# Kernel tuning notes

Hardware: AMD Instinct MI355X
Metric: run time of the kernel (lower is better)

## Reference

```python
import jax, jax.numpy as jnp
import numpy as np

N_NODES = 100000
IN_DIM = 128
HID = 128
N_REL = 2
N_EDGES = 500000


def setup_inputs() -> dict:
    key = jax.random.key(0)
    ks = jax.random.split(key, 12)
    x = jax.random.normal(ks[0], (N_NODES, IN_DIM), dtype=jnp.float32)
    edge_index = jax.random.randint(ks[1], (2, N_EDGES), 0, N_NODES, dtype=jnp.int64)
    edge_type = jax.random.randint(ks[2], (N_EDGES,), 0, N_REL, dtype=jnp.int64)
    def w(k, shape, fan_in):
        return jax.random.normal(k, shape, dtype=jnp.float32) / np.sqrt(fan_in)
    return {
        "x": x,
        "edge_index": edge_index,
        "edge_type": edge_type,
        "W_rel1": w(ks[3], (N_REL, IN_DIM, HID), IN_DIM),
        "W_root1": w(ks[4], (IN_DIM, HID), IN_DIM),
        "b1": jnp.zeros((HID,), jnp.float32),
        "W_rel2": w(ks[5], (N_REL, HID, HID), HID),
        "W_root2": w(ks[6], (HID, HID), HID),
        "b2": jnp.zeros((HID,), jnp.float32),
        "Wc": w(ks[7], (HID, 2), HID),
        "bc": jnp.zeros((2,), jnp.float32),
    }


def rgcn_conv(x, src, dst, edge_type, W_rel, W_root, b, n_nodes):
    """PyG RGCNConv: out_i = x_i @ W_root + b + sum_r mean_{j in N_r(i)} x_j @ W_r."""
    out = x @ W_root + b
    for r in range(W_rel.shape[0]):  # small fixed relation count
        mask = (edge_type == r).astype(x.dtype)  # [E]
        xr = x @ W_rel[r]                         # [N, dout] transform-then-gather
        msg = xr[src] * mask[:, None]             # [E, dout]
        agg = jax.ops.segment_sum(msg, dst, num_segments=n_nodes)   # [N, dout]
        cnt = jax.ops.segment_sum(mask, dst, num_segments=n_nodes)  # [N]
        out = out + agg / jnp.maximum(cnt, 1.0)[:, None]            # mean aggr
    return out


def reference(x, edge_index, edge_type, W_rel1, W_root1, b1, W_rel2, W_root2, b2, Wc, bc):
    n = x.shape[0]
    src, dst = edge_index[0], edge_index[1]
    h = rgcn_conv(x, src, dst, edge_type, W_rel1, W_root1, b1, n)
    h = jax.nn.relu(h)
    # dropout is identity at inference (training=False)
    h = rgcn_conv(h, src, dst, edge_type, W_rel2, W_root2, b2, n)
    h = jax.nn.relu(h)
    logits = h @ Wc + bc
    return logits
```

## Files before the change

### kernel.cpp

```cpp
#include <hip/hip_runtime.h>
#include <hip/hip_fp16.h>

#define N_NODES 100000
#define PAD_N   100096
#define IN_DIM 128
#define HID 128
#define N_REL 2
#define N_EDGES 500000
#define M_SEG (N_REL * N_NODES)
#define SCAN_BLK 1024
#define SCAN_NB ((M_SEG + SCAN_BLK - 1) / SCAN_BLK)

#define CVT_BLOCKS 12500
#define PACK_BLOCKS 48
#define HIST_BLOCKS 1954

#define GB_EDGES 48

typedef __attribute__((ext_vector_type(8))) _Float16 half8;
typedef __attribute__((ext_vector_type(4))) float float4v;

__device__ __forceinline__ unsigned short f2h(float f) {
    return __half_as_ushort(__float2half(f));
}

__global__ __launch_bounds__(256) void prep_kernel(
    const float* __restrict__ X, unsigned short* __restrict__ Xb,
    const float* __restrict__ Wroot1, const float* __restrict__ Wrel1,
    const float* __restrict__ Wroot2, const float* __restrict__ Wrel2,
    unsigned short* __restrict__ Wp,
    const int* __restrict__ ei, const int* __restrict__ et,
    unsigned* __restrict__ cnt)
{
    int bid = blockIdx.x;
    if (bid < CVT_BLOCKS) {
        int i = bid * 256 + threadIdx.x;
        if (i >= N_NODES * IN_DIM / 4) return;
        float4 v = ((const float4*)X)[i];
        ushort4 o;
        o.x = f2h(v.x); o.y = f2h(v.y); o.z = f2h(v.z); o.w = f2h(v.w);
        ((ushort4*)Xb)[i] = o;
    } else if (bid < CVT_BLOCKS + PACK_BLOCKS) {
        int tid = (bid - CVT_BLOCKS) * 256 + threadIdx.x;
        int layer = tid / 6144;
        int rem   = tid % 6144;
        int ks    = rem / 512;
        int rem2  = rem % 512;
        int nt    = rem2 / 64;
        int lane  = rem2 % 64;
        int seg = ks >> 2;
        int kl  = (ks & 3) * 32 + (lane >> 4) * 8;
        int chan = layer ? (nt * 16 + (lane & 15)) : ((lane & 15) * 8 + nt);
        const float* Wroot = layer ? Wroot2 : Wroot1;
        const float* Wrel  = layer ? Wrel2  : Wrel1;
        const float* W = (seg == 0) ? Wroot : (Wrel + (size_t)(seg - 1) * 128 * 128);
        unsigned short* dst = Wp + (size_t)tid * 8;
        #pragma unroll
        for (int j = 0; j < 8; ++j)
            dst[j] = f2h(W[(size_t)(kl + j) * 128 + chan]);
    } else {
        int e = (bid - CVT_BLOCKS - PACK_BLOCKS) * 256 + threadIdx.x;
        if (e >= N_EDGES) return;
        int dst = ei[N_EDGES + e];
        int r = et[e];
        atomicAdd(cnt + (size_t)r * N_NODES + dst, 1u);
    }
}

__global__ __launch_bounds__(256) void scan1_kernel(
    const unsigned* __restrict__ cnt,
    unsigned* __restrict__ rs, unsigned* __restrict__ bsums)
{
    __shared__ unsigned sdata[256];
    int t = threadIdx.x;
    int base = blockIdx.x * SCAN_BLK + t * 4;
    unsigned v[4]; unsigned s = 0;
    #pragma unroll
    for (int j = 0; j < 4; ++j) {
        v[j] = (base + j < M_SEG) ? cnt[base + j] : 0u;
        s += v[j];
    }
    sdata[t] = s;
    __syncthreads();
    #pragma unroll
    for (int off = 1; off < 256; off <<= 1) {
        unsigned x = (t >= off) ? sdata[t - off] : 0u;
        __syncthreads();
        if (t >= off) sdata[t] += x;
        __syncthreads();
    }
    unsigned excl = (t > 0) ? sdata[t - 1] : 0u;
    if (t == 255) bsums[blockIdx.x] = sdata[255];
    unsigned run = excl;
    #pragma unroll
    for (int j = 0; j < 4; ++j) {
        if (base + j < M_SEG) rs[base + j] = run;
        run += v[j];
    }
}

__global__ __launch_bounds__(256) void scan3_kernel(
    unsigned* __restrict__ rs, const unsigned* __restrict__ bsums,
    unsigned* __restrict__ cursor)
{
    __shared__ unsigned sdata[256];
    int t = threadIdx.x;
    sdata[t] = (t < SCAN_NB) ? bsums[t] : 0u;
    __syncthreads();
    #pragma unroll
    for (int off = 1; off < 256; off <<= 1) {
        unsigned x = (t >= off) ? sdata[t - off] : 0u;
        __syncthreads();
        if (t >= off) sdata[t] += x;
        __syncthreads();
    }
    int i = blockIdx.x * blockDim.x + t;
    if (i < M_SEG) {
        int b = i >> 10;
        unsigned add = (b > 0) ? sdata[b - 1] : 0u;
        unsigned v = rs[i] + add;
        rs[i] = v;
        cursor[i] = v;
    }
    if (i == 0) rs[M_SEG] = N_EDGES;
}

__global__ __launch_bounds__(256) void fill_kernel(
    const int* __restrict__ ei, const int* __restrict__ et,
    unsigned* __restrict__ cursor, unsigned* __restrict__ csr)
{
    int e = blockIdx.x * blockDim.x + threadIdx.x;
    if (e >= N_EDGES) return;
    int src = ei[e];
    int dst = ei[N_EDGES + e];
    int r = et[e];
    unsigned pos = atomicAdd(cursor + (size_t)r * N_NODES + dst, 1u);
    csr[pos] = (unsigned)src;
}

template <bool FINAL>
__global__ __launch_bounds__(256) void gemm_kernel(
    const unsigned short* __restrict__ Xin,
    const unsigned* __restrict__ rs,
    const unsigned* __restrict__ csr,
    const unsigned short* __restrict__ Wp,
    const float* __restrict__ bias,
    unsigned short* __restrict__ Hout,
    const float* __restrict__ Wc,
    const float* __restrict__ bc,
    float* __restrict__ Out)
{
    __shared__ __align__(16) unsigned char lds_raw[49152];

    const int t    = threadIdx.x;
    const int w    = t >> 6;
    const int lane = t & 63;
    const int l15  = lane & 15;
    const int quad = lane >> 4;
    const int rowbase = blockIdx.x * 64 + w * 16;
    const int koff = quad * 8;
    unsigned char* myBuf = lds_raw + w * (GB_EDGES * 256);
    unsigned short* ldsB = (unsigned short*)lds_raw;

    const uint4* __restrict__ X4 = (const uint4*)Xin;

    const unsigned short* aBase = Xin + (size_t)(rowbase + l15) * 128 + koff;
    half8 ax[4];
    #pragma unroll
    for (int ksl = 0; ksl < 4; ++ksl)
        ax[ksl] = *(const half8*)(aBase + ksl * 32);

    __half2 a2[2][4][4];
    #pragma unroll
    for (int r = 0; r < 2; ++r)
        #pragma unroll
        for (int ksl = 0; ksl < 4; ++ksl)
            #pragma unroll
            for (int j = 0; j < 4; ++j)
                a2[r][ksl][j] = __float2half2_rn(0.f);

    const int node = rowbase + l15;
    float inv_[2] = {1.f, 1.f};

    auto volley = [&](unsigned idv, unsigned cnt) {
        #pragma unroll
        for (int i = 0; i < 12; ++i) {
            if ((unsigned)(i * 4) < cnt) {
                unsigned id = (unsigned)__shfl((int)idv, i * 4 + (lane >> 4), 64);
                unsigned eL = (unsigned)(i * 4) + (unsigned)(lane >> 4);
                unsigned cg = (unsigned)(lane & 15) ^ (eL & 7u);
                const unsigned short* gp =
                    (const unsigned short*)(X4 + ((size_t)id << 4) + cg);
                __builtin_amdgcn_global_load_lds(
                    (const __attribute__((address_space(1))) unsigned int*)gp,
                    (__attribute__((address_space(3))) unsigned int*)(myBuf + i * 1024),
                    16, 0, 0);
            }
        }
    };

    auto accum = [&](int r, unsigned base, unsigned cnt, unsigned st, unsigned en) {
        unsigned lo = st > base ? st : base;
        unsigned hiB = base + cnt;
        unsigned hi = en < hiB ? en : hiB;
        for (unsigned p = lo; p < hi; ++p) {
            unsigned eL = p - base;
            const unsigned char* rowb = myBuf + eL * 256;
            #pragma unroll
            for (int ksl = 0; ksl < 4; ++ksl) {
                unsigned pos = ((unsigned)(ksl * 4 + quad)) ^ (eL & 7u);
                half8 h = *(const half8*)(rowb + pos * 16);
                #pragma unroll
                for (int j = 0; j < 4; ++j)
                    a2[r][ksl][j] = __hadd2(a2[r][ksl][j],
                                            ((const __half2*)&h)[j]);
            }
        }
    };

    if (rowbase < N_NODES) {
        unsigned S0 = rs[rowbase],               E0 = rs[rowbase + 16];
        unsigned st0 = rs[node],                 en0 = rs[node + 1];
        unsigned S1 = rs[N_NODES + rowbase],     E1 = rs[N_NODES + rowbase + 16];
        unsigned st1 = rs[N_NODES + node],       en1 = rs[N_NODES + node + 1];
        unsigned d0 = en0 - st0; inv_[0] = 1.0f / (float)(d0 ? d0 : 1u);
        unsigned d1 = en1 - st1; inv_[1] = 1.0f / (float)(d1 ? d1 : 1u);

        unsigned c0 = E0 - S0; if (c0 > GB_EDGES) c0 = GB_EDGES;
        unsigned c1 = E1 - S1; if (c1 > GB_EDGES) c1 = GB_EDGES;

        unsigned q0 = S0 + (unsigned)lane;
        unsigned idv0 = (E0 > S0) ? csr[q0 < E0 ? q0 : E0 - 1u] : 0u;
        unsigned q1 = S1 + (unsigned)lane;
        unsigned idv1 = (E1 > S1) ? csr[q1 < E1 ? q1 : E1 - 1u] : 0u;

        volley(idv0, c0);
        asm volatile("s_waitcnt vmcnt(0)" ::: "memory");
        __builtin_amdgcn_sched_barrier(0);
        accum(0, S0, c0, st0, en0);

        asm volatile("s_waitcnt lgkmcnt(0)" ::: "memory");
        __builtin_amdgcn_sched_barrier(0);
        volley(idv1, c1);
        asm volatile("s_waitcnt vmcnt(0)" ::: "memory");
        __builtin_amdgcn_sched_barrier(0);
        accum(1, S1, c1, st1, en1);

        #pragma unroll
        for (int r = 0; r < 2; ++r) {
            unsigned S  = r ? S1  : S0;
            unsigned E  = r ? E1  : E0;
            unsigned st = r ? st1 : st0;
            unsigned en = r ? en1 : en0;
            for (unsigned base = S + GB_EDGES; base < E; base += GB_EDGES) {
                unsigned cnt = E - base;
                if (cnt > GB_EDGES) cnt = GB_EDGES;
                unsigned q = base + (unsigned)lane;
                unsigned idv = csr[q < E ? q : E - 1u];
                asm volatile("s_waitcnt lgkmcnt(0)" ::: "memory");
                __builtin_amdgcn_sched_barrier(0);
                volley(idv, cnt);
                asm volatile("s_waitcnt vmcnt(0)" ::: "memory");
                __builtin_amdgcn_sched_barrier(0);
                accum(r, base, cnt, st, en);
            }
        }
    }

    half8 ag[2][4];
    #pragma unroll
    for (int r = 0; r < 2; ++r) {
        __half2 s2 = __float2half2_rn(inv_[r]);
        #pragma unroll
        for (int ksl = 0; ksl < 4; ++ksl) {
            half8 h;
            #pragma unroll
            for (int j = 0; j < 4; ++j)
                ((__half2*)&h)[j] = __hmul2(a2[r][ksl][j], s2);
            ag[r][ksl] = h;
        }
    }

    __syncthreads();

    auto stage = [&](int ph, int buf) {
        #pragma unroll
        for (int fi = 0; fi < 6; ++fi) {
            int f  = fi * 4 + w;
            int sl = f >> 3;
            int nt = f & 7;
            int ks = ph * 3 + sl;
            const unsigned short* g = Wp + ((size_t)(ks * 8 + nt) * 64 + lane) * 8;
            unsigned short* l = ldsB + (size_t)buf * 12288 + (size_t)(sl * 8 + nt) * 512;
            __builtin_amdgcn_global_load_lds(
                (const __attribute__((address_space(1))) unsigned int*)g,
                (__attribute__((address_space(3))) unsigned int*)l, 16, 0, 0);
        }
    };

    float4v acc[8];
    #pragma unroll
    for (int nt = 0; nt < 8; ++nt) {
        float bv = FINAL ? bias[nt * 16 + l15] : bias[l15 * 8 + nt];
        acc[nt] = float4v{bv, bv, bv, bv};
    }

    stage(0, 0);
    __syncthreads();

    #pragma unroll
    for (int ph = 0; ph < 4; ++ph) {
        if (ph < 3) stage(ph + 1, (ph + 1) & 1);
        #pragma unroll
        for (int sl = 0; sl < 3; ++sl) {
            int ks = ph * 3 + sl;
            half8 b[8];
            #pragma unroll
            for (int nt = 0; nt < 8; ++nt)
                b[nt] = *(const half8*)(ldsB + (size_t)(ph & 1) * 12288 +
                                        (size_t)(sl * 8 + nt) * 512 + lane * 8);
            half8 A = (ks < 4) ? ax[ks] : ag[(ks >> 2) - 1][ks & 3];
            #pragma unroll
            for (int nt = 0; nt < 8; ++nt)
                acc[nt] = __builtin_amdgcn_mfma_f32_16x16x32_f16(A, b[nt], acc[nt], 0, 0, 0);
        }
        __syncthreads();
    }

    if (!FINAL) {
        #pragma unroll
        for (int rr = 0; rr < 4; ++rr) {
            int n2 = rowbase + quad * 4 + rr;
            __half2 hv[4];
            #pragma unroll
            for (int j = 0; j < 4; ++j)
                hv[j] = __floats2half2_rn(fmaxf(acc[2 * j][rr], 0.f),
                                          fmaxf(acc[2 * j + 1][rr], 0.f));
            *(uint4*)(Hout + (size_t)n2 * 128 + l15 * 8) = *(const uint4*)hv;
        }
    } else {
        float wc0[8], wc1[8];
        #pragma unroll
        for (int nt = 0; nt < 8; ++nt) {
            wc0[nt] = Wc[(nt * 16 + l15) * 2 + 0];
            wc1[nt] = Wc[(nt * 16 + l15) * 2 + 1];
        }
        float b0 = bc[0], b1 = bc[1];
        #pragma unroll
        for (int rr = 0; rr < 4; ++rr) {
            float l0 = 0.f, l1 = 0.f;
            #pragma unroll
            for (int nt = 0; nt < 8; ++nt) {
                float h = fmaxf(acc[nt][rr], 0.f);
                l0 += h * wc0[nt];
                l1 += h * wc1[nt];
            }
            #pragma unroll
            for (int off = 8; off > 0; off >>= 1) {
                l0 += __shfl_down(l0, off, 16);
                l1 += __shfl_down(l1, off, 16);
            }
            int n2 = rowbase + quad * 4 + rr;
            if (l15 == 0 && n2 < N_NODES) {
                Out[(size_t)n2 * 2 + 0] = l0 + b0;
                Out[(size_t)n2 * 2 + 1] = l1 + b1;
            }
        }
    }
}

extern "C" void kernel_launch(void* const* d_in, const int* in_sizes, int n_in,
                              void* d_out, int out_size, void* d_ws, size_t ws_size,
                              hipStream_t stream)
{
    const float* x      = (const float*)d_in[0];
    const int*   ei     = (const int*)d_in[1];
    const int*   et     = (const int*)d_in[2];
    const float* Wrel1  = (const float*)d_in[3];
    const float* Wroot1 = (const float*)d_in[4];
    const float* b1     = (const float*)d_in[5];
    const float* Wrel2  = (const float*)d_in[6];
    const float* Wroot2 = (const float*)d_in[7];
    const float* b2     = (const float*)d_in[8];
    const float* Wc     = (const float*)d_in[9];
    const float* bc     = (const float*)d_in[10];
    float* out = (float*)d_out;

    char* ws = (char*)d_ws;
    size_t off = 0;
    auto alloc = [&](size_t bytes) {
        void* p = ws + off;
        off += (bytes + 255) & ~(size_t)255;
        return p;
    };
    unsigned short* xb    = (unsigned short*)alloc((size_t)PAD_N * IN_DIM * 2);
    unsigned short* h1b   = (unsigned short*)alloc((size_t)PAD_N * HID * 2);
    unsigned short* Wp    = (unsigned short*)alloc((size_t)2 * 12 * 8 * 64 * 8 * 2);
    unsigned*       rs    = (unsigned*)alloc((size_t)(M_SEG + 1) * 4);
    unsigned*       cursor= (unsigned*)alloc((size_t)M_SEG * 4);
    unsigned*       bsums = (unsigned*)alloc(256 * 4);
    unsigned*       csr   = (unsigned*)alloc((size_t)N_EDGES * 4);

    const int edge_blocks = (N_EDGES + 255) / 256;
    const int seg_blocks  = (M_SEG + 255) / 256;
    const int gemm_blocks = PAD_N / 64;
    const int prep_blocks = CVT_BLOCKS + PACK_BLOCKS + HIST_BLOCKS;

    hipMemsetAsync(cursor, 0, (size_t)M_SEG * 4, stream);
    prep_kernel<<<prep_blocks, 256, 0, stream>>>(
        x, xb, Wroot1, Wrel1, Wroot2, Wrel2, Wp, ei, et, cursor);
    scan1_kernel<<<SCAN_NB, 256, 0, stream>>>(cursor, rs, bsums);
    scan3_kernel<<<seg_blocks, 256, 0, stream>>>(rs, bsums, cursor);
    fill_kernel<<<edge_blocks, 256, 0, stream>>>(ei, et, cursor, csr);

    gemm_kernel<false><<<gemm_blocks, 256, 0, stream>>>(
        xb, rs, csr, Wp, b1, h1b, nullptr, nullptr, nullptr);

    gemm_kernel<true><<<gemm_blocks, 256, 0, stream>>>(
        h1b, rs, csr, Wp + (size_t)12 * 8 * 64 * 8, b2, nullptr, Wc, bc, out);
}
```

Before: 241.9 us.

## Double-buffer edge gathers into LDS halves to overlap loads with accumulation

Splits each wave's 48-edge LDS gather buffer into two 24-edge halves. The per-relation gather volleys are now issued unconditionally, with clamped source indices, so that vmcnt(6) waits let one half be accumulated while the next half's global_load_lds requests are still in flight. The goal is to hide gather latency behind fp16 accumulation instead of stalling on a full vmcnt(0) per relation. The cost is redundant loads for low-degree nodes, because all 6 loads per half are always issued, plus smaller 24-edge chunks in the overflow loop.

```diff
diff --git a/kernel.cpp b/kernel.cpp
--- a/kernel.cpp
+++ b/kernel.cpp
@@ -160,6 +160,8 @@
     const int rowbase = blockIdx.x * 64 + w * 16;
     const int koff = quad * 8;
     unsigned char* myBuf = lds_raw + w * (GB_EDGES * 256);
+    unsigned char* halfA = myBuf;
+    unsigned char* halfB = myBuf + 24 * 256;
     unsigned short* ldsB = (unsigned short*)lds_raw;
 
     const uint4* __restrict__ X4 = (const uint4*)Xin;
@@ -182,30 +184,33 @@
     const int node = rowbase + l15;
     float inv_[2] = {1.f, 1.f};
 
-    auto volley = [&](unsigned idv, unsigned cnt) {
-        #pragma unroll
-        for (int i = 0; i < 12; ++i) {
-            if ((unsigned)(i * 4) < cnt) {
-                unsigned id = (unsigned)__shfl((int)idv, i * 4 + (lane >> 4), 64);
-                unsigned eL = (unsigned)(i * 4) + (unsigned)(lane >> 4);
-                unsigned cg = (unsigned)(lane & 15) ^ (eL & 7u);
-                const unsigned short* gp =
-                    (const unsigned short*)(X4 + ((size_t)id << 4) + cg);
-                __builtin_amdgcn_global_load_lds(
-                    (const __attribute__((address_space(1))) unsigned int*)gp,
-                    (__attribute__((address_space(3))) unsigned int*)(myBuf + i * 1024),
-                    16, 0, 0);
-            }
+    auto volley6 = [&](unsigned idv, unsigned off, unsigned cm, unsigned char* half) {
+        #pragma unroll
+        for (int i = 0; i < 6; ++i) {
+            unsigned eL = (unsigned)(i * 4) + (unsigned)(lane >> 4);
+            unsigned srcIdx = off + eL;
+            unsigned clampv = cm ? cm - 1u : 0u;
+            srcIdx = srcIdx < cm ? srcIdx : clampv;
+            unsigned id = (unsigned)__shfl((int)idv, (int)srcIdx, 64);
+            unsigned cg = (unsigned)(lane & 15) ^ (eL & 7u);
+            const unsigned short* gp =
+                (const unsigned short*)(X4 + ((size_t)id << 4) + cg);
+            __builtin_amdgcn_global_load_lds(
+                (const __attribute__((address_space(1))) unsigned int*)gp,
+                (__attribute__((address_space(3))) unsigned int*)(half + i * 1024),
+                16, 0, 0);
         }
     };
 
-    auto accum = [&](int r, unsigned base, unsigned cnt, unsigned st, unsigned en) {
-        unsigned lo = st > base ? st : base;
-        unsigned hiB = base + cnt;
+    auto accumB = [&](int r, unsigned S, unsigned off, unsigned lim,
+                      unsigned st, unsigned en, const unsigned char* half) {
+        unsigned gbase = S + off;
+        unsigned lo = st > gbase ? st : gbase;
+        unsigned hiB = S + lim;
         unsigned hi = en < hiB ? en : hiB;
         for (unsigned p = lo; p < hi; ++p) {
-            unsigned eL = p - base;
-            const unsigned char* rowb = myBuf + eL * 256;
+            unsigned eL = p - gbase;
+            const unsigned char* rowb = half + eL * 256;
             #pragma unroll
             for (int ksl = 0; ksl < 4; ++ksl) {
                 unsigned pos = ((unsigned)(ksl * 4 + quad)) ^ (eL & 7u);
@@ -226,25 +231,40 @@
         unsigned d0 = en0 - st0; inv_[0] = 1.0f / (float)(d0 ? d0 : 1u);
         unsigned d1 = en1 - st1; inv_[1] = 1.0f / (float)(d1 ? d1 : 1u);
 
-        unsigned c0 = E0 - S0; if (c0 > GB_EDGES) c0 = GB_EDGES;
-        unsigned c1 = E1 - S1; if (c1 > GB_EDGES) c1 = GB_EDGES;
+        unsigned c0 = E0 - S0, c1 = E1 - S1;
+        unsigned m0 = c0 > GB_EDGES ? GB_EDGES : c0;
+        unsigned m1 = c1 > GB_EDGES ? GB_EDGES : c1;
+        unsigned l0a = m0 > 24u ? 24u : m0;
+        unsigned l1a = m1 > 24u ? 24u : m1;
 
         unsigned q0 = S0 + (unsigned)lane;
-        unsigned idv0 = (E0 > S0) ? csr[q0 < E0 ? q0 : E0 - 1u] : 0u;
+        unsigned idv0 = c0 ? csr[q0 < E0 ? q0 : E0 - 1u] : 0u;
         unsigned q1 = S1 + (unsigned)lane;
-        unsigned idv1 = (E1 > S1) ? csr[q1 < E1 ? q1 : E1 - 1u] : 0u;
-
-        volley(idv0, c0);
+        unsigned idv1 = c1 ? csr[q1 < E1 ? q1 : E1 - 1u] : 0u;
+
         asm volatile("s_waitcnt vmcnt(0)" ::: "memory");
         __builtin_amdgcn_sched_barrier(0);
-        accum(0, S0, c0, st0, en0);
-
+
+        volley6(idv0, 0u,  m0, halfA);
+        volley6(idv0, 24u, m0, halfB);
+        asm volatile("s_waitcnt vmcnt(6)" ::: "memory");
+        __builtin_amdgcn_sched_barrier(0);
+        accumB(0, S0, 0u, l0a, st0, en0, halfA);
         asm volatile("s_waitcnt lgkmcnt(0)" ::: "memory");
         __builtin_amdgcn_sched_barrier(0);
-        volley(idv1, c1);
+        volley6(idv1, 0u, m1, halfA);
+        asm volatile("s_waitcnt vmcnt(6)" ::: "memory");
+        __builtin_amdgcn_sched_barrier(0);
+        accumB(0, S0, 24u, m0, st0, en0, halfB);
+        asm volatile("s_waitcnt lgkmcnt(0)" ::: "memory");
+        __builtin_amdgcn_sched_barrier(0);
+        volley6(idv1, 24u, m1, halfB);
+        asm volatile("s_waitcnt vmcnt(6)" ::: "memory");
+        __builtin_amdgcn_sched_barrier(0);
+        accumB(1, S1, 0u, l1a, st1, en1, halfA);
         asm volatile("s_waitcnt vmcnt(0)" ::: "memory");
         __builtin_amdgcn_sched_barrier(0);
-        accum(1, S1, c1, st1, en1);
+        accumB(1, S1, 24u, m1, st1, en1, halfB);
 
         #pragma unroll
         for (int r = 0; r < 2; ++r) {
@@ -252,17 +272,17 @@
             unsigned E  = r ? E1  : E0;
             unsigned st = r ? st1 : st0;
             unsigned en = r ? en1 : en0;
-            for (unsigned base = S + GB_EDGES; base < E; base += GB_EDGES) {
+            for (unsigned base = S + GB_EDGES; base < E; base += 24u) {
                 unsigned cnt = E - base;
-                if (cnt > GB_EDGES) cnt = GB_EDGES;
+                if (cnt > 24u) cnt = 24u;
                 unsigned q = base + (unsigned)lane;
                 unsigned idv = csr[q < E ? q : E - 1u];
                 asm volatile("s_waitcnt lgkmcnt(0)" ::: "memory");
                 __builtin_amdgcn_sched_barrier(0);
-                volley(idv, cnt);
+                volley6(idv, 0u, cnt, halfA);
                 asm volatile("s_waitcnt vmcnt(0)" ::: "memory");
                 __builtin_amdgcn_sched_barrier(0);
-                accum(r, base, cnt, st, en);
+                accumB(r, base, 0u, cnt, st, en, halfA);
             }
         }
     }
```

New measurement: 233.3 us. 3.5% less time.
